# Performance work log

Hardware: AMD Instinct MI355X
Metric: run time of the kernel (lower is better)

## Reference

```python
import jax, jax.numpy as jnp
import numpy as np

B, T, I, R, H = 8, 2048, 128, 1024, 256
LEAKY = 1.0           # leaky_rate
SPECTRAL_RADIUS = 0.9


def setup_inputs() -> dict:
    key = jax.random.key(0)
    ks = jax.random.split(key, 8)
    u = jax.random.normal(ks[0], (B, T, I), dtype=jnp.float32)
    # ESN cell weights (fixed random reservoir)
    w_in = jax.random.normal(ks[1], (R, I), dtype=jnp.float32) * (1.0 / np.sqrt(I))  # input_scaling=1
    w = jax.random.normal(ks[2], (R, R), dtype=jnp.float32) * (SPECTRAL_RADIUS / np.sqrt(R))
    w_bias = jnp.zeros((R,), dtype=jnp.float32)  # bias_scaling=0
    # PCA stand-in: fixed linear projection reservoir -> pca space
    w_pca = jax.random.normal(ks[3], (R, H), dtype=jnp.float32) * (1.0 / np.sqrt(R))
    # gate weights: torch.rand -> uniform [0,1)
    wzp = jax.random.uniform(ks[4], (H, H), dtype=jnp.float32)
    wzh = jax.random.uniform(ks[5], (H, H), dtype=jnp.float32)
    bz = jax.random.uniform(ks[6], (H,), dtype=jnp.float32)
    return {"u": u, "w_in": w_in, "w": w, "w_bias": w_bias,
            "w_pca": w_pca, "wzp": wzp, "wzh": wzh, "bz": bz}


def reference(u, w_in, w, w_bias, w_pca, wzp, wzh, bz):
    Bn = u.shape[0]
    Rd = w.shape[0]
    Hd = bz.shape[0]
    # Precompute input drive for all timesteps: (T, B, R)
    uin = jnp.swapaxes(jnp.einsum('bti,ri->btr', u, w_in) + w_bias, 0, 1)

    # ESN leaky reservoir recurrence: x_t = (1-a)x_{t-1} + a*tanh(W_in u_t + W x_{t-1} + b)
    def res_step(x, u_t):
        x_new = (1.0 - LEAKY) * x + LEAKY * jnp.tanh(u_t + x @ w.T)
        return x_new, x_new

    x0 = jnp.zeros((Bn, Rd), dtype=u.dtype)
    _, res_states = jax.lax.scan(res_step, x0, uin)          # (T, B, R)

    # PCA projection (linear stand-in for fitted IncrementalPCA)
    pca_states = jnp.einsum('tbr,rh->tbh', res_states, w_pca)  # (T, B, H)

    # Gated recurrence: z_t = sigmoid(Wzp p_t + Wzh h_{t-1} + bz); h_t = (1-z)*h + z*p
    def gate_step(h, p):
        z = jax.nn.sigmoid(p @ wzp.T + h @ wzh.T + bz)
        h_new = (1.0 - z) * h + z * p
        return h_new, h_new

    h0 = jnp.zeros((Bn, Hd), dtype=u.dtype)  # per-batch reset_hidden()
    _, hidden_states = jax.lax.scan(gate_step, h0, pca_states)  # (T, B, H)
    return jnp.swapaxes(hidden_states, 0, 1)                    # (B, T, H)
```

## Files before the change

### kernel.cpp

```cpp
#include <hip/hip_runtime.h>
#include <hip/hip_bf16.h>

#define TSTEPS 2048
#define NCHAIN 8
#define RDIM 1024
#define IDIM 128
#define HDIM 256
#define NB 16
#define NTHR 512
#define NBLOCKS (NB * NCHAIN)

typedef unsigned long long u64_t;

__device__ __forceinline__ float aload(const float* p) {
  return __hip_atomic_load(p, __ATOMIC_RELAXED, __HIP_MEMORY_SCOPE_AGENT);
}
__device__ __forceinline__ void astore(float* p, float v) {
  __hip_atomic_store(p, v, __ATOMIC_RELAXED, __HIP_MEMORY_SCOPE_AGENT);
}
__device__ __forceinline__ float2 aload2(const float* p) {
  u64_t q = __hip_atomic_load(reinterpret_cast<const u64_t*>(p),
                              __ATOMIC_RELAXED, __HIP_MEMORY_SCOPE_AGENT);
  union { u64_t u; float2 f; } c; c.u = q;
  return c.f;
}

__device__ __forceinline__ float wave_sum(float v) {
  v += __shfl_xor(v, 1);
  v += __shfl_xor(v, 2);
  v += __shfl_xor(v, 4);
  v += __shfl_xor(v, 8);
  v += __shfl_xor(v, 16);
  v += __shfl_xor(v, 32);
  return v;
}

__device__ __forceinline__ void gbar(unsigned* cnt, unsigned target) {
  asm volatile("s_waitcnt vmcnt(0) lgkmcnt(0)" ::: "memory");
  __syncthreads();
  if (threadIdx.x == 0) {
    __hip_atomic_fetch_add(cnt, 1u, __ATOMIC_RELAXED, __HIP_MEMORY_SCOPE_AGENT);
    unsigned it = 0;
    while (__hip_atomic_load(cnt, __ATOMIC_RELAXED, __HIP_MEMORY_SCOPE_AGENT) < target) {
      __builtin_amdgcn_s_sleep(1);
      if (++it > (1u << 15)) break;
    }
  }
  __syncthreads();
}

__global__ __launch_bounds__(NTHR, 2) void esn_fused(
    const float* __restrict__ u, const float* __restrict__ w_in,
    const float* __restrict__ w, const float* __restrict__ w_bias,
    const float* __restrict__ w_pca, const float* __restrict__ wzp,
    const float* __restrict__ wzh, const float* __restrict__ bz,
    float* __restrict__ out,
    float* __restrict__ x_buf,
    float* __restrict__ p_buf,
    float* __restrict__ h_buf,
    unsigned* __restrict__ barr)
{
  const int bid = blockIdx.x;
  const int chain = bid & 7;
  const int sub = bid >> 3;
  const int tid = threadIdx.x;
  const int wave = tid >> 6;
  const int lane = tid & 63;
  unsigned* cnt = barr + chain * 64;

  const int rrow0 = sub * 64 + wave * 8;
  float4 WA[8][4];
  #pragma unroll
  for (int j = 0; j < 8; ++j)
    #pragma unroll
    for (int i = 0; i < 4; ++i)
      WA[j][i] = *reinterpret_cast<const float4*>(
          w + (size_t)(rrow0 + j) * RDIM + lane * 16 + i * 4);
  float2 Wi[8];
  #pragma unroll
  for (int j = 0; j < 8; ++j)
    Wi[j] = *reinterpret_cast<const float2*>(w_in + (size_t)(rrow0 + j) * IDIM + lane * 2);
  const float wb = (lane < 8) ? w_bias[rrow0 + lane] : 0.f;

  const int pcol0 = sub * 16 + wave * 2;
  float Wp[2][16];
  #pragma unroll
  for (int j = 0; j < 2; ++j)
    #pragma unroll
    for (int k = 0; k < 16; ++k)
      Wp[j][k] = w_pca[(size_t)(lane * 16 + k) * HDIM + pcol0 + j];

  const int grow0 = sub * 16 + wave * 2;
  float4 Zp[2], Zh[2];
  #pragma unroll
  for (int j = 0; j < 2; ++j) {
    Zp[j] = *reinterpret_cast<const float4*>(wzp + (size_t)(grow0 + j) * HDIM + lane * 4);
    Zh[j] = *reinterpret_cast<const float4*>(wzh + (size_t)(grow0 + j) * HDIM + lane * 4);
  }
  const float bzr = (lane < 2) ? bz[grow0 + lane] : 0.f;

  for (int s = 0; s < TSTEPS + 2; ++s) {
    float xc[16];
    const bool xc_valid = (s >= 1 && s <= TSTEPS);
    if (xc_valid) {
      const float* xp = x_buf + ((((s - 1) & 1) * NCHAIN) + chain) * RDIM + lane * 16;
      #pragma unroll
      for (int k = 0; k < 8; ++k) {
        float2 f = aload2(xp + 2 * k);
        xc[2 * k] = f.x;
        xc[2 * k + 1] = f.y;
      }
    }

    if (s < TSTEPS) {
      float acc[8];
      float2 uu = *reinterpret_cast<const float2*>(
          u + ((size_t)chain * TSTEPS + s) * IDIM + lane * 2);
      #pragma unroll
      for (int j = 0; j < 8; ++j) acc[j] = Wi[j].x * uu.x + Wi[j].y * uu.y;
      if (s > 0) {
        #pragma unroll
        for (int j = 0; j < 8; ++j) {
          float a = acc[j];
          #pragma unroll
          for (int i = 0; i < 4; ++i) {
            a += WA[j][i].x * xc[i * 4 + 0];
            a += WA[j][i].y * xc[i * 4 + 1];
            a += WA[j][i].z * xc[i * 4 + 2];
            a += WA[j][i].w * xc[i * 4 + 3];
          }
          acc[j] = a;
        }
      }
      #pragma unroll
      for (int j = 0; j < 8; ++j) acc[j] = wave_sum(acc[j]);
      float v = acc[0];
      #pragma unroll
      for (int j = 1; j < 8; ++j) v = (lane == j) ? acc[j] : v;
      if (lane < 8)
        astore(x_buf + (((s & 1) * NCHAIN) + chain) * RDIM + rrow0 + lane,
               tanhf(v + wb));
    }

    if (xc_valid) {
      const int t = s - 1;
      float a0 = 0.f, a1 = 0.f;
      #pragma unroll
      for (int k = 0; k < 16; ++k) { a0 += Wp[0][k] * xc[k]; a1 += Wp[1][k] * xc[k]; }
      a0 = wave_sum(a0);
      a1 = wave_sum(a1);
      float v = (lane == 1) ? a1 : a0;
      if (lane < 2)
        astore(p_buf + (((t & 1) * NCHAIN) + chain) * HDIM + pcol0 + lane, v);
    }

    if (s >= 2) {
      const int t = s - 2;
      const float* pv = p_buf + (((t & 1) * NCHAIN) + chain) * HDIM;
      const float* hv = h_buf + ((((t - 1) & 1) * NCHAIN) + chain) * HDIM;
      float pc[4], hc[4];
      {
        float2 f0 = aload2(pv + lane * 4), f1 = aload2(pv + lane * 4 + 2);
        pc[0] = f0.x; pc[1] = f0.y; pc[2] = f1.x; pc[3] = f1.y;
      }
      if (t > 0) {
        float2 f0 = aload2(hv + lane * 4), f1 = aload2(hv + lane * 4 + 2);
        hc[0] = f0.x; hc[1] = f0.y; hc[2] = f1.x; hc[3] = f1.y;
      } else {
        hc[0] = hc[1] = hc[2] = hc[3] = 0.f;
      }
      float a0 = Zp[0].x * pc[0] + Zp[0].y * pc[1] + Zp[0].z * pc[2] + Zp[0].w * pc[3]
               + Zh[0].x * hc[0] + Zh[0].y * hc[1] + Zh[0].z * hc[2] + Zh[0].w * hc[3];
      float a1 = Zp[1].x * pc[0] + Zp[1].y * pc[1] + Zp[1].z * pc[2] + Zp[1].w * pc[3]
               + Zh[1].x * hc[0] + Zh[1].y * hc[1] + Zh[1].z * hc[2] + Zh[1].w * hc[3];
      a0 = wave_sum(a0);
      a1 = wave_sum(a1);
      float v = (lane == 1) ? a1 : a0;
      if (lane < 2) {
        const int row = grow0 + lane;
        float z = 1.f / (1.f + expf(-(v + bzr)));
        float pt = aload(pv + row);
        float hp = (t > 0) ? aload(hv + row) : 0.f;
        float hnew = hp + z * (pt - hp);
        astore(h_buf + (((t & 1) * NCHAIN) + chain) * HDIM + row, hnew);
        out[((size_t)chain * TSTEPS + t) * HDIM + row] = hnew;
      }
    }

    if (s <= TSTEPS) gbar(cnt, (unsigned)(s + 1) * NB);
  }
}

extern "C" void kernel_launch(void* const* d_in, const int* in_sizes, int n_in,
                              void* d_out, int out_size, void* d_ws, size_t ws_size,
                              hipStream_t stream) {
  const float* ptrs[8] = {nullptr};
  const int want[8] = {TSTEPS * NCHAIN * IDIM,
                       RDIM * IDIM,
                       RDIM * RDIM,
                       RDIM,
                       RDIM * HDIM,
                       HDIM * HDIM,
                       HDIM * HDIM,
                       HDIM};
  if (n_in == 8) {
    int used[8] = {0};
    for (int k = 0; k < 8; ++k) {
      for (int i = 0; i < n_in; ++i) {
        if (!used[i] && in_sizes[i] == want[k]) {
          ptrs[k] = (const float*)d_in[i];
          used[i] = 1;
          break;
        }
      }
    }
  }
  bool ok = true;
  for (int k = 0; k < 8; ++k) ok = ok && (ptrs[k] != nullptr);
  if (!ok)
    for (int k = 0; k < 8; ++k) ptrs[k] = (const float*)d_in[k];

  float* out = (float*)d_out;

  float* x_buf = (float*)d_ws;
  float* p_buf = x_buf + 2 * NCHAIN * RDIM;
  float* h_buf = p_buf + 2 * NCHAIN * HDIM;
  unsigned* barr = (unsigned*)(h_buf + 2 * NCHAIN * HDIM);
  size_t zero_floats =
      (size_t)(2 * NCHAIN * RDIM + 2 * NCHAIN * HDIM * 2 + NCHAIN * 64);
  if (ws_size < zero_floats * 4) return;
  hipMemsetAsync(d_ws, 0, zero_floats * 4, stream);

  esn_fused<<<dim3(NBLOCKS), dim3(NTHR), 0, stream>>>(
      ptrs[0], ptrs[1], ptrs[2], ptrs[3], ptrs[4], ptrs[5], ptrs[6], ptrs[7],
      out, x_buf, p_buf, h_buf, barr);
}
```

Measured before the change: 13.71 ms.

## Replace per-step counter barrier with epoch-tagged data slots in a ring

Drops the global atomic counter barrier between timesteps. Each published value (reservoir state, PCA projection, hidden state) is now a 64-bit word that pairs the float with its step tag, held in a 4-deep ring. Dedicated waves spin until every tag matches, then stage the values into LDS for the block. This removes the per-step fetch_add and sleep-polling round trip, so blocks can run ahead on independent stages. The cost is double-width traffic, busy polling by three waves, and reliance on 64-bit atomic stores pairing tag and data.

```diff
diff --git a/kernel.cpp b/kernel.cpp
--- a/kernel.cpp
+++ b/kernel.cpp
@@ -9,19 +9,22 @@
 #define NB 16
 #define NTHR 512
 #define NBLOCKS (NB * NCHAIN)
+#define RINGD 4
 
 typedef unsigned long long u64_t;
 
-__device__ __forceinline__ float aload(const float* p) {
+__device__ __forceinline__ u64_t aload64(const u64_t* p) {
   return __hip_atomic_load(p, __ATOMIC_RELAXED, __HIP_MEMORY_SCOPE_AGENT);
 }
-__device__ __forceinline__ void astore(float* p, float v) {
+__device__ __forceinline__ void astore64(u64_t* p, u64_t v) {
   __hip_atomic_store(p, v, __ATOMIC_RELAXED, __HIP_MEMORY_SCOPE_AGENT);
 }
-__device__ __forceinline__ float2 aload2(const float* p) {
-  u64_t q = __hip_atomic_load(reinterpret_cast<const u64_t*>(p),
-                              __ATOMIC_RELAXED, __HIP_MEMORY_SCOPE_AGENT);
-  union { u64_t u; float2 f; } c; c.u = q;
+__device__ __forceinline__ u64_t pack_fe(float f, unsigned e) {
+  union { float f; unsigned u; } c; c.f = f;
+  return ((u64_t)e << 32) | (u64_t)c.u;
+}
+__device__ __forceinline__ float unpack_f(u64_t v) {
+  union { unsigned u; float f; } c; c.u = (unsigned)(v & 0xffffffffu);
   return c.f;
 }
 
@@ -35,30 +38,15 @@
   return v;
 }
 
-__device__ __forceinline__ void gbar(unsigned* cnt, unsigned target) {
-  asm volatile("s_waitcnt vmcnt(0) lgkmcnt(0)" ::: "memory");
-  __syncthreads();
-  if (threadIdx.x == 0) {
-    __hip_atomic_fetch_add(cnt, 1u, __ATOMIC_RELAXED, __HIP_MEMORY_SCOPE_AGENT);
-    unsigned it = 0;
-    while (__hip_atomic_load(cnt, __ATOMIC_RELAXED, __HIP_MEMORY_SCOPE_AGENT) < target) {
-      __builtin_amdgcn_s_sleep(1);
-      if (++it > (1u << 15)) break;
-    }
-  }
-  __syncthreads();
-}
-
 __global__ __launch_bounds__(NTHR, 2) void esn_fused(
     const float* __restrict__ u, const float* __restrict__ w_in,
     const float* __restrict__ w, const float* __restrict__ w_bias,
     const float* __restrict__ w_pca, const float* __restrict__ wzp,
     const float* __restrict__ wzh, const float* __restrict__ bz,
     float* __restrict__ out,
-    float* __restrict__ x_buf,
-    float* __restrict__ p_buf,
-    float* __restrict__ h_buf,
-    unsigned* __restrict__ barr)
+    u64_t* __restrict__ xslot,
+    u64_t* __restrict__ pslot,
+    u64_t* __restrict__ hslot)
 {
   const int bid = blockIdx.x;
   const int chain = bid & 7;
@@ -66,7 +54,10 @@
   const int tid = threadIdx.x;
   const int wave = tid >> 6;
   const int lane = tid & 63;
-  unsigned* cnt = barr + chain * 64;
+
+  __shared__ float LX[2][RDIM];
+  __shared__ float LP[2][HDIM];
+  __shared__ float LH[2][HDIM];
 
   const int rrow0 = sub * 64 + wave * 8;
   float4 WA[8][4];
@@ -99,17 +90,67 @@
   }
   const float bzr = (lane < 2) ? bz[grow0 + lane] : 0.f;
 
-  for (int s = 0; s < TSTEPS + 2; ++s) {
+  for (int s = 0; s <= TSTEPS + 1; ++s) {
+    const int par = s & 1;
+
+    if (wave == 0 && s >= 1 && s <= TSTEPS) {
+      const u64_t* xs = xslot + ((size_t)((s - 1) & 3) * NCHAIN + chain) * RDIM + lane * 16;
+      #pragma unroll
+      for (int half = 0; half < 2; ++half) {
+        u64_t v[8];
+        unsigned it = 0;
+        for (;;) {
+          #pragma unroll
+          for (int k = 0; k < 8; ++k) v[k] = aload64(xs + half * 8 + k);
+          bool ok = true;
+          #pragma unroll
+          for (int k = 0; k < 8; ++k) ok &= ((unsigned)(v[k] >> 32) == (unsigned)s);
+          if (__all(ok ? 1 : 0)) break;
+          if (++it > (1u << 16)) break;
+        }
+        #pragma unroll
+        for (int k = 0; k < 8; ++k)
+          LX[par][(half * 8 + k) * 64 + lane] = unpack_f(v[k]);
+      }
+    }
+    if (wave == 1 && s >= 2 && s <= TSTEPS + 1) {
+      const u64_t* ps = pslot + ((size_t)((s - 2) & 3) * NCHAIN + chain) * HDIM + lane * 4;
+      u64_t v[4];
+      unsigned it = 0;
+      for (;;) {
+        #pragma unroll
+        for (int k = 0; k < 4; ++k) v[k] = aload64(ps + k);
+        bool ok = true;
+        #pragma unroll
+        for (int k = 0; k < 4; ++k) ok &= ((unsigned)(v[k] >> 32) == (unsigned)(s - 1));
+        if (__all(ok ? 1 : 0)) break;
+        if (++it > (1u << 16)) break;
+      }
+      #pragma unroll
+      for (int k = 0; k < 4; ++k) LP[par][k * 64 + lane] = unpack_f(v[k]);
+    }
+    if (wave == 2 && s >= 3 && s <= TSTEPS + 1) {
+      const u64_t* hs = hslot + ((size_t)((s - 3) & 3) * NCHAIN + chain) * HDIM + lane * 4;
+      u64_t v[4];
+      unsigned it = 0;
+      for (;;) {
+        #pragma unroll
+        for (int k = 0; k < 4; ++k) v[k] = aload64(hs + k);
+        bool ok = true;
+        #pragma unroll
+        for (int k = 0; k < 4; ++k) ok &= ((unsigned)(v[k] >> 32) == (unsigned)(s - 2));
+        if (__all(ok ? 1 : 0)) break;
+        if (++it > (1u << 16)) break;
+      }
+      #pragma unroll
+      for (int k = 0; k < 4; ++k) LH[par][k * 64 + lane] = unpack_f(v[k]);
+    }
+    __syncthreads();
+
     float xc[16];
-    const bool xc_valid = (s >= 1 && s <= TSTEPS);
-    if (xc_valid) {
-      const float* xp = x_buf + ((((s - 1) & 1) * NCHAIN) + chain) * RDIM + lane * 16;
-      #pragma unroll
-      for (int k = 0; k < 8; ++k) {
-        float2 f = aload2(xp + 2 * k);
-        xc[2 * k] = f.x;
-        xc[2 * k + 1] = f.y;
-      }
+    if (s >= 1 && s <= TSTEPS) {
+      #pragma unroll
+      for (int k = 0; k < 16; ++k) xc[k] = LX[par][k * 64 + lane];
     }
 
     if (s < TSTEPS) {
@@ -138,11 +179,11 @@
       #pragma unroll
       for (int j = 1; j < 8; ++j) v = (lane == j) ? acc[j] : v;
       if (lane < 8)
-        astore(x_buf + (((s & 1) * NCHAIN) + chain) * RDIM + rrow0 + lane,
-               tanhf(v + wb));
-    }
-
-    if (xc_valid) {
+        astore64(xslot + ((size_t)(s & 3) * NCHAIN + chain) * RDIM + rrow0 + lane,
+                 pack_fe(tanhf(v + wb), (unsigned)(s + 1)));
+    }
+
+    if (s >= 1 && s <= TSTEPS) {
       const int t = s - 1;
       float a0 = 0.f, a1 = 0.f;
       #pragma unroll
@@ -151,24 +192,17 @@
       a1 = wave_sum(a1);
       float v = (lane == 1) ? a1 : a0;
       if (lane < 2)
-        astore(p_buf + (((t & 1) * NCHAIN) + chain) * HDIM + pcol0 + lane, v);
+        astore64(pslot + ((size_t)(t & 3) * NCHAIN + chain) * HDIM + pcol0 + lane,
+                 pack_fe(v, (unsigned)(t + 1)));
     }
 
     if (s >= 2) {
       const int t = s - 2;
-      const float* pv = p_buf + (((t & 1) * NCHAIN) + chain) * HDIM;
-      const float* hv = h_buf + ((((t - 1) & 1) * NCHAIN) + chain) * HDIM;
       float pc[4], hc[4];
-      {
-        float2 f0 = aload2(pv + lane * 4), f1 = aload2(pv + lane * 4 + 2);
-        pc[0] = f0.x; pc[1] = f0.y; pc[2] = f1.x; pc[3] = f1.y;
-      }
-      if (t > 0) {
-        float2 f0 = aload2(hv + lane * 4), f1 = aload2(hv + lane * 4 + 2);
-        hc[0] = f0.x; hc[1] = f0.y; hc[2] = f1.x; hc[3] = f1.y;
-      } else {
-        hc[0] = hc[1] = hc[2] = hc[3] = 0.f;
-      }
+      #pragma unroll
+      for (int e = 0; e < 4; ++e) pc[e] = LP[par][e * 64 + lane];
+      #pragma unroll
+      for (int e = 0; e < 4; ++e) hc[e] = (t > 0) ? LH[par][e * 64 + lane] : 0.f;
       float a0 = Zp[0].x * pc[0] + Zp[0].y * pc[1] + Zp[0].z * pc[2] + Zp[0].w * pc[3]
                + Zh[0].x * hc[0] + Zh[0].y * hc[1] + Zh[0].z * hc[2] + Zh[0].w * hc[3];
       float a1 = Zp[1].x * pc[0] + Zp[1].y * pc[1] + Zp[1].z * pc[2] + Zp[1].w * pc[3]
@@ -179,15 +213,14 @@
       if (lane < 2) {
         const int row = grow0 + lane;
         float z = 1.f / (1.f + expf(-(v + bzr)));
-        float pt = aload(pv + row);
-        float hp = (t > 0) ? aload(hv + row) : 0.f;
+        float pt = LP[par][(row & 3) * 64 + (row >> 2)];
+        float hp = (t > 0) ? LH[par][(row & 3) * 64 + (row >> 2)] : 0.f;
         float hnew = hp + z * (pt - hp);
-        astore(h_buf + (((t & 1) * NCHAIN) + chain) * HDIM + row, hnew);
+        astore64(hslot + ((size_t)(t & 3) * NCHAIN + chain) * HDIM + row,
+                 pack_fe(hnew, (unsigned)(t + 1)));
         out[((size_t)chain * TSTEPS + t) * HDIM + row] = hnew;
       }
     }
-
-    if (s <= TSTEPS) gbar(cnt, (unsigned)(s + 1) * NB);
   }
 }
 
@@ -222,16 +255,14 @@
 
   float* out = (float*)d_out;
 
-  float* x_buf = (float*)d_ws;
-  float* p_buf = x_buf + 2 * NCHAIN * RDIM;
-  float* h_buf = p_buf + 2 * NCHAIN * HDIM;
-  unsigned* barr = (unsigned*)(h_buf + 2 * NCHAIN * HDIM);
-  size_t zero_floats =
-      (size_t)(2 * NCHAIN * RDIM + 2 * NCHAIN * HDIM * 2 + NCHAIN * 64);
-  if (ws_size < zero_floats * 4) return;
-  hipMemsetAsync(d_ws, 0, zero_floats * 4, stream);
+  u64_t* xslot = (u64_t*)d_ws;
+  u64_t* pslot = xslot + (size_t)RINGD * NCHAIN * RDIM;
+  u64_t* hslot = pslot + (size_t)RINGD * NCHAIN * HDIM;
+  size_t total_u64 = (size_t)RINGD * NCHAIN * (RDIM + 2 * HDIM);
+  if (ws_size < total_u64 * 8) return;
+  hipMemsetAsync(d_ws, 0, total_u64 * 8, stream);
 
   esn_fused<<<dim3(NBLOCKS), dim3(NTHR), 0, stream>>>(
       ptrs[0], ptrs[1], ptrs[2], ptrs[3], ptrs[4], ptrs[5], ptrs[6], ptrs[7],
-      out, x_buf, p_buf, h_buf, barr);
-}
+      out, xslot, pslot, hslot);
+}
```

New measurement: 15.62 ms. 13.9% more time.
